# Optimization experiments

Measured on AMD Instinct MI355X. Metric: run time of the kernel, lower is better.

Reference implementation:

```python
import jax
import jax.numpy as jnp
from jax import lax
import numpy as np

B, N, NPOINT, NSAMPLE, C = 8, 8192, 2048, 32, 64
RADIUS = 0.2
BIG = jnp.float32(1e10)


def setup_inputs() -> dict:
    key = jax.random.key(0)
    ks = jax.random.split(key, 8)
    xyz = jax.random.uniform(ks[0], (B, N, 3), dtype=jnp.float32)          # points in unit cube
    features = jax.random.normal(ks[1], (B, C, N), dtype=jnp.float32)
    w1 = jax.random.normal(ks[2], (64, C + 3), dtype=jnp.float32) * 0.1
    b1 = jnp.zeros((64,), jnp.float32)
    w2 = jax.random.normal(ks[3], (64, 64), dtype=jnp.float32) * 0.1
    b2 = jnp.zeros((64,), jnp.float32)
    w3 = jax.random.normal(ks[4], (128, 64), dtype=jnp.float32) * 0.1
    b3 = jnp.zeros((128,), jnp.float32)
    return {"xyz": xyz, "features": features, "w1": w1, "b1": b1,
            "w2": w2, "b2": b2, "w3": w3, "b3": b3}


def _fps(xyz, npoint):
    """Furthest point sampling. xyz: (B,N,3) -> idx (B,npoint) int32."""
    def one(pts):  # (N,3)
        n = pts.shape[0]
        def step(carry, _):
            dist, far = carry
            d = jnp.sum((pts - pts[far]) ** 2, axis=-1)    # (N,)
            dist = jnp.minimum(dist, d)
            nxt = jnp.argmax(dist).astype(jnp.int32)
            return (dist, nxt), far
        init = (jnp.full((n,), BIG, pts.dtype), jnp.int32(0))
        _, idx = lax.scan(step, init, None, length=npoint)
        return idx
    return jax.vmap(one)(xyz)


def _ball_query(xyz, new_xyz, radius, nsample):
    """xyz (B,N,3), new_xyz (B,S,3) -> idx (B,S,nsample) int32, pointnet2 semantics:
    first nsample in-radius points in index order; pad with first hit."""
    n = xyz.shape[1]
    d2 = (jnp.sum(new_xyz ** 2, -1)[:, :, None]
          + jnp.sum(xyz ** 2, -1)[:, None, :]
          - 2.0 * jnp.einsum("bsd,bnd->bsn", new_xyz, xyz))  # (B,S,N)
    mask = d2 < radius * radius
    keys = jnp.where(mask, jnp.arange(n, dtype=jnp.int32)[None, None, :], jnp.int32(n))
    idx = jnp.sort(keys, axis=-1)[..., :nsample]             # (B,S,nsample)
    first = idx[..., :1]
    idx = jnp.where(idx >= n, first, idx)
    idx = jnp.where(idx >= n, 0, idx)                        # degenerate: no neighbor at all
    return idx


def _conv_bn_relu(h, w, b):
    # 1x1 Conv2d over (B, Cin, S, ns) with folded BN -> ReLU
    return jax.nn.relu(jnp.einsum("oc,bcps->bops", w, h) + b[None, :, None, None])


def _forward(xyz, features, w1, b1, w2, b2, w3, b3):
    fps_idx = _fps(xyz, NPOINT)                                          # (B,S)
    new_xyz = jnp.take_along_axis(xyz, fps_idx[:, :, None], axis=1)      # (B,S,3)
    idx = _ball_query(xyz, new_xyz, RADIUS, NSAMPLE)                     # (B,S,ns)
    b, s, ns = idx.shape
    flat = idx.reshape(b, s * ns)
    grouped_xyz = jnp.take_along_axis(xyz, flat[:, :, None], axis=1).reshape(b, s, ns, 3)
    grouped_xyz = grouped_xyz - new_xyz[:, :, None, :]                   # center
    grouped_xyz = jnp.transpose(grouped_xyz, (0, 3, 1, 2))               # (B,3,S,ns)
    grouped_feat = jnp.take_along_axis(features, flat[:, None, :], axis=2).reshape(b, C, s, ns)
    h = jnp.concatenate([grouped_xyz, grouped_feat], axis=1)             # (B,3+C,S,ns)
    h = _conv_bn_relu(h, w1, b1)
    h = _conv_bn_relu(h, w2, b2)
    h = _conv_bn_relu(h, w3, b3)
    new_features = jnp.max(h, axis=-1)                                   # (B,128,S)
    return new_xyz, new_features


def reference(xyz, features, w1, b1, w2, b2, w3, b3):
    return _forward(xyz, features, w1, b1, w2, b2, w3, b3)
```

## Files before the change

### kernel.cpp

```cpp
#include <hip/hip_runtime.h>
#include <stdint.h>

#define NB 8
#define NN 8192
#define NP 2048
#define NSAMP 32
#define NC 64

__global__ __launch_bounds__(256) void prep_kernel(
    const float* __restrict__ w1, const float* __restrict__ w2,
    const float* __restrict__ w3, float* __restrict__ w1t,
    float* __restrict__ w2t, float* __restrict__ w3t)
{
    int j = blockIdx.x * 256 + threadIdx.x;
    if (j < 64*67) { int o = j / 67, k = j % 67; w1t[k*64 + o] = w1[j]; }
    int j2 = j - 64*67;
    if (j2 >= 0 && j2 < 64*64) { int o = j2 >> 6, k = j2 & 63; w2t[k*64 + o] = w2[j2]; }
    int j3 = j2 - 64*64;
    if (j3 >= 0 && j3 < 128*64) { int o = j3 >> 6, k = j3 & 63; w3t[k*128 + o] = w3[j3]; }
}

#define DPP_MAXF(m, CTRL) do { \
    int _s = __builtin_amdgcn_update_dpp(__float_as_int(m), __float_as_int(m), \
                                         CTRL, 0xf, 0xf, false); \
    float _f = __int_as_float(_s); \
    m = fmaxf(m, _f); } while (0)

#define DPP_MINI(c, CTRL) do { \
    int _s = __builtin_amdgcn_update_dpp(c, c, CTRL, 0xf, 0xf, false); \
    c = (_s < c) ? _s : c; } while (0)

__global__ __launch_bounds__(256, 1) void fps_kernel(
    const float* __restrict__ xyz, int* __restrict__ fps_idx,
    float* __restrict__ out_newxyz)
{
#pragma clang fp contract(off)
    __shared__ float sxyz[NN * 3];
    __shared__ float bv[2][4];
    __shared__ int   bix[2][4];

    const int b = blockIdx.x;
    const int t = threadIdx.x;
    const int lane = t & 63;
    const int w = t >> 6;
    const float* base = xyz + (size_t)b * NN * 3;

    for (int i = t; i < NN * 3 / 4; i += 256)
        ((float4*)sxyz)[i] = ((const float4*)base)[i];
    __syncthreads();

    const int p0 = t * 32;
    float px[32], py[32], pz[32], dist[32];
    #pragma unroll
    for (int j = 0; j < 32; j++) {
        px[j] = sxyz[(p0 + j) * 3 + 0];
        py[j] = sxyz[(p0 + j) * 3 + 1];
        pz[j] = sxyz[(p0 + j) * 3 + 2];
        dist[j] = 1e10f;
    }

    int far = 0;
    for (int k = 0; k < NP; k++) {
        float fx = sxyz[far * 3 + 0];
        float fy = sxyz[far * 3 + 1];
        float fz = sxyz[far * 3 + 2];
        if (t == 0) {
            fps_idx[b * NP + k] = far;
            out_newxyz[((size_t)b * NP + k) * 3 + 0] = fx;
            out_newxyz[((size_t)b * NP + k) * 3 + 1] = fy;
            out_newxyz[((size_t)b * NP + k) * 3 + 2] = fz;
        }

        float bva0 = -1.f, bva1 = -1.f, bva2 = -1.f, bva3 = -1.f;
        int   bja0 = 0,    bja1 = 0,    bja2 = 0,    bja3 = 0;
        #pragma unroll
        for (int j8 = 0; j8 < 8; j8++) {
            {   int j = j8;
                float dx = px[j] - fx, dy = py[j] - fy, dz = pz[j] - fz;
                float d = (dx*dx + dy*dy) + dz*dz;
                float nd = fminf(dist[j], d); dist[j] = nd;
                if (nd > bva0) { bva0 = nd; bja0 = p0 + j; } }
            {   int j = 8 + j8;
                float dx = px[j] - fx, dy = py[j] - fy, dz = pz[j] - fz;
                float d = (dx*dx + dy*dy) + dz*dz;
                float nd = fminf(dist[j], d); dist[j] = nd;
                if (nd > bva1) { bva1 = nd; bja1 = p0 + j; } }
            {   int j = 16 + j8;
                float dx = px[j] - fx, dy = py[j] - fy, dz = pz[j] - fz;
                float d = (dx*dx + dy*dy) + dz*dz;
                float nd = fminf(dist[j], d); dist[j] = nd;
                if (nd > bva2) { bva2 = nd; bja2 = p0 + j; } }
            {   int j = 24 + j8;
                float dx = px[j] - fx, dy = py[j] - fy, dz = pz[j] - fz;
                float d = (dx*dx + dy*dy) + dz*dz;
                float nd = fminf(dist[j], d); dist[j] = nd;
                if (nd > bva3) { bva3 = nd; bja3 = p0 + j; } }
        }
        float best = bva0; int bj = bja0;
        if (bva1 > best) { best = bva1; bj = bja1; }
        if (bva2 > best) { best = bva2; bj = bja2; }
        if (bva3 > best) { best = bva3; bj = bja3; }

        float m = best;
        DPP_MAXF(m, 0x111); DPP_MAXF(m, 0x112); DPP_MAXF(m, 0x114);
        DPP_MAXF(m, 0x118); DPP_MAXF(m, 0x142); DPP_MAXF(m, 0x143);
        float wm = __int_as_float(__builtin_amdgcn_readlane(__float_as_int(m), 63));

        int cand = (best == wm) ? bj : 0x7FFFFFFF;
        DPP_MINI(cand, 0x111); DPP_MINI(cand, 0x112); DPP_MINI(cand, 0x114);
        DPP_MINI(cand, 0x118); DPP_MINI(cand, 0x142); DPP_MINI(cand, 0x143);
        int widx = __builtin_amdgcn_readlane(cand, 63);

        if (lane == 0) { bv[k & 1][w] = wm; bix[k & 1][w] = widx; }
        __syncthreads();

        float v0 = bv[k & 1][0], v1 = bv[k & 1][1];
        float v2 = bv[k & 1][2], v3 = bv[k & 1][3];
        int   i0 = bix[k & 1][0], i1 = bix[k & 1][1];
        int   i2 = bix[k & 1][2], i3 = bix[k & 1][3];
        float gv = v0; int gi = i0;
        if (v1 > gv) { gv = v1; gi = i1; }
        if (v2 > gv) { gv = v2; gi = i2; }
        if (v3 > gv) { gv = v3; gi = i3; }
        far = gi;
    }
}

__global__ __launch_bounds__(64) void fused_kernel(
    const float* __restrict__ xyz, const float* __restrict__ features,
    const int* __restrict__ fps_idx,
    const float* __restrict__ w1t, const float* __restrict__ b1,
    const float* __restrict__ w2t, const float* __restrict__ b2,
    const float* __restrict__ w3t, const float* __restrict__ b3,
    float* __restrict__ out_feat)
{
#pragma clang fp contract(off)
    constexpr int XP = 36;
    __shared__ __align__(16) float Xs[67 * XP];
    __shared__ __align__(16) float Hs[64 * XP];
    __shared__ int ids[NSAMP];

    const int q = blockIdx.x;
    const int b = q >> 11, s = q & (NP - 1);
    const int lane = threadIdx.x;
    const float* base = xyz + (size_t)b * NN * 3;

    int qi = fps_idx[q];
    float qx = base[qi*3+0], qy = base[qi*3+1], qz = base[qi*3+2];
    float qq = (qx*qx + qy*qy) + qz*qz;
    const float RR = 0.04f;

    int have = 0, first = 0;
    for (int c = 0; c < NN / 64; c++) {
        int p = c * 64 + lane;
        float px = base[p*3+0], py = base[p*3+1], pz = base[p*3+2];
        float pp  = (px*px + py*py) + pz*pz;
        float dot = fmaf(qz, pz, fmaf(qy, py, qx*px));
        float d2  = (qq + pp) - 2.0f*dot;
        bool pred = d2 < RR;
        unsigned long long m = __ballot(pred);
        if (have == 0 && m) first = c * 64 + (int)__builtin_ctzll(m);
        if (pred) {
            int rank = have + (int)__popcll(m & ((1ULL << lane) - 1ULL));
            if (rank < NSAMP) ids[rank] = p;
        }
        have += (int)__popcll(m);
        if (have >= NSAMP) break;
    }
    if (lane < NSAMP && lane >= have) ids[lane] = first;
    __syncthreads();

    if (lane < NSAMP) {
        int id = ids[lane];
        Xs[0*XP + lane] = base[id*3+0] - qx;
        Xs[1*XP + lane] = base[id*3+1] - qy;
        Xs[2*XP + lane] = base[id*3+2] - qz;
    }
    {
        const float* frow = features + ((size_t)b * NC + lane) * NN;
        #pragma unroll
        for (int n0 = 0; n0 < NSAMP; n0 += 4) {
            float4 v;
            v.x = frow[ids[n0+0]];
            v.y = frow[ids[n0+1]];
            v.z = frow[ids[n0+2]];
            v.w = frow[ids[n0+3]];
            *(float4*)&Xs[(3 + lane) * XP + n0] = v;
        }
    }
    __syncthreads();

    float acc[32];
    {
        float bias = b1[lane];
        #pragma unroll
        for (int n = 0; n < 32; n++) acc[n] = bias;
        for (int k = 0; k < 67; k++) {
            float w = w1t[k*64 + lane];
            const float4* xr = (const float4*)&Xs[k * XP];
            #pragma unroll
            for (int n4 = 0; n4 < 8; n4++) {
                float4 xv = xr[n4];
                acc[n4*4+0] = fmaf(w, xv.x, acc[n4*4+0]);
                acc[n4*4+1] = fmaf(w, xv.y, acc[n4*4+1]);
                acc[n4*4+2] = fmaf(w, xv.z, acc[n4*4+2]);
                acc[n4*4+3] = fmaf(w, xv.w, acc[n4*4+3]);
            }
        }
        #pragma unroll
        for (int n0 = 0; n0 < 32; n0 += 4) {
            float4 v;
            v.x = fmaxf(acc[n0+0], 0.f); v.y = fmaxf(acc[n0+1], 0.f);
            v.z = fmaxf(acc[n0+2], 0.f); v.w = fmaxf(acc[n0+3], 0.f);
            *(float4*)&Hs[lane * XP + n0] = v;
        }
    }
    __syncthreads();
    {
        float bias = b2[lane];
        #pragma unroll
        for (int n = 0; n < 32; n++) acc[n] = bias;
        for (int k = 0; k < 64; k++) {
            float w = w2t[k*64 + lane];
            const float4* xr = (const float4*)&Hs[k * XP];
            #pragma unroll
            for (int n4 = 0; n4 < 8; n4++) {
                float4 xv = xr[n4];
                acc[n4*4+0] = fmaf(w, xv.x, acc[n4*4+0]);
                acc[n4*4+1] = fmaf(w, xv.y, acc[n4*4+1]);
                acc[n4*4+2] = fmaf(w, xv.z, acc[n4*4+2]);
                acc[n4*4+3] = fmaf(w, xv.w, acc[n4*4+3]);
            }
        }
        __syncthreads();
        #pragma unroll
        for (int n0 = 0; n0 < 32; n0 += 4) {
            float4 v;
            v.x = fmaxf(acc[n0+0], 0.f); v.y = fmaxf(acc[n0+1], 0.f);
            v.z = fmaxf(acc[n0+2], 0.f); v.w = fmaxf(acc[n0+3], 0.f);
            *(float4*)&Xs[lane * XP + n0] = v;
        }
    }
    __syncthreads();
    {
        float accA[32], accB[32];
        float ba = b3[lane], bb = b3[lane + 64];
        #pragma unroll
        for (int n = 0; n < 32; n++) { accA[n] = ba; accB[n] = bb; }
        for (int k = 0; k < 64; k++) {
            float wa = w3t[k*128 + lane];
            float wb = w3t[k*128 + lane + 64];
            const float4* xr = (const float4*)&Xs[k * XP];
            #pragma unroll
            for (int n4 = 0; n4 < 8; n4++) {
                float4 xv = xr[n4];
                accA[n4*4+0] = fmaf(wa, xv.x, accA[n4*4+0]);
                accA[n4*4+1] = fmaf(wa, xv.y, accA[n4*4+1]);
                accA[n4*4+2] = fmaf(wa, xv.z, accA[n4*4+2]);
                accA[n4*4+3] = fmaf(wa, xv.w, accA[n4*4+3]);
                accB[n4*4+0] = fmaf(wb, xv.x, accB[n4*4+0]);
                accB[n4*4+1] = fmaf(wb, xv.y, accB[n4*4+1]);
                accB[n4*4+2] = fmaf(wb, xv.z, accB[n4*4+2]);
                accB[n4*4+3] = fmaf(wb, xv.w, accB[n4*4+3]);
            }
        }
        float mA = accA[0], mB = accB[0];
        #pragma unroll
        for (int n = 1; n < 32; n++) { mA = fmaxf(mA, accA[n]); mB = fmaxf(mB, accB[n]); }
        mA = fmaxf(mA, 0.f); mB = fmaxf(mB, 0.f);
        out_feat[((size_t)b*128 + lane)      * NP + s] = mA;
        out_feat[((size_t)b*128 + lane + 64) * NP + s] = mB;
    }
}

extern "C" void kernel_launch(void* const* d_in, const int* in_sizes, int n_in,
                              void* d_out, int out_size, void* d_ws, size_t ws_size,
                              hipStream_t stream)
{
    const float* xyz      = (const float*)d_in[0];
    const float* features = (const float*)d_in[1];
    const float* w1 = (const float*)d_in[2];
    const float* b1 = (const float*)d_in[3];
    const float* w2 = (const float*)d_in[4];
    const float* b2 = (const float*)d_in[5];
    const float* w3 = (const float*)d_in[6];
    const float* b3 = (const float*)d_in[7];

    float* out        = (float*)d_out;
    float* out_newxyz = out;
    float* out_feat   = out + NB * NP * 3;

    char* ws = (char*)d_ws;
    int*   fps_idx = (int*)(ws + 0);
    float* w1t     = (float*)(ws + 65536);
    float* w2t     = (float*)(ws + 82688);
    float* w3t     = (float*)(ws + 99072);

    prep_kernel<<<65, 256, 0, stream>>>(w1, w2, w3, w1t, w2t, w3t);
    fps_kernel<<<NB, 256, 0, stream>>>(xyz, fps_idx, out_newxyz);
    fused_kernel<<<NB * NP, 64, 0, stream>>>(xyz, features, fps_idx,
                                             w1t, b1, w2t, b2, w3t, b3, out_feat);
}
```

Measured before the change: 2.382 ms.

## Widen FPS block to 512 threads with packed float2 math and max-then-find argmax

The furthest point sampling kernel now runs 512 threads per block, each owning 16 points instead of 32, which halves the serial per-iteration work in this latency-bound loop. Coordinates and distances are held as two-wide float vectors so the distance computation can use packed FP32 instructions. The per-thread argmax is split into a plain max reduction followed by an equality scan for the lowest matching index. The cost is a cross-wave reduction over 8 waves instead of 4, and the block barrier per iteration now synchronises more waves.

```diff
diff --git a/kernel.cpp b/kernel.cpp
--- a/kernel.cpp
+++ b/kernel.cpp
@@ -6,6 +6,8 @@
 #define NP 2048
 #define NSAMP 32
 #define NC 64
+
+typedef float v2f __attribute__((ext_vector_type(2)));
 
 __global__ __launch_bounds__(256) void prep_kernel(
     const float* __restrict__ w1, const float* __restrict__ w2,
@@ -30,14 +32,14 @@
     int _s = __builtin_amdgcn_update_dpp(c, c, CTRL, 0xf, 0xf, false); \
     c = (_s < c) ? _s : c; } while (0)
 
-__global__ __launch_bounds__(256, 1) void fps_kernel(
+__global__ __launch_bounds__(512) void fps_kernel(
     const float* __restrict__ xyz, int* __restrict__ fps_idx,
     float* __restrict__ out_newxyz)
 {
 #pragma clang fp contract(off)
     __shared__ float sxyz[NN * 3];
-    __shared__ float bv[2][4];
-    __shared__ int   bix[2][4];
+    __shared__ float bv[2][8];
+    __shared__ int   bix[2][8];
 
     const int b = blockIdx.x;
     const int t = threadIdx.x;
@@ -45,18 +47,19 @@
     const int w = t >> 6;
     const float* base = xyz + (size_t)b * NN * 3;
 
-    for (int i = t; i < NN * 3 / 4; i += 256)
+    for (int i = t; i < NN * 3 / 4; i += 512)
         ((float4*)sxyz)[i] = ((const float4*)base)[i];
     __syncthreads();
 
-    const int p0 = t * 32;
-    float px[32], py[32], pz[32], dist[32];
+    const int p0 = t * 16;
+    v2f X[8], Y[8], Z[8], D[8];
     #pragma unroll
-    for (int j = 0; j < 32; j++) {
-        px[j] = sxyz[(p0 + j) * 3 + 0];
-        py[j] = sxyz[(p0 + j) * 3 + 1];
-        pz[j] = sxyz[(p0 + j) * 3 + 2];
-        dist[j] = 1e10f;
+    for (int j = 0; j < 8; j++) {
+        int pa = p0 + 2*j, pb = p0 + 2*j + 1;
+        X[j] = (v2f){ sxyz[pa*3+0], sxyz[pb*3+0] };
+        Y[j] = (v2f){ sxyz[pa*3+1], sxyz[pb*3+1] };
+        Z[j] = (v2f){ sxyz[pa*3+2], sxyz[pb*3+2] };
+        D[j] = (v2f){ 1e10f, 1e10f };
     }
 
     int far = 0;
@@ -71,42 +74,35 @@
             out_newxyz[((size_t)b * NP + k) * 3 + 2] = fz;
         }
 
-        float bva0 = -1.f, bva1 = -1.f, bva2 = -1.f, bva3 = -1.f;
-        int   bja0 = 0,    bja1 = 0,    bja2 = 0,    bja3 = 0;
-        #pragma unroll
-        for (int j8 = 0; j8 < 8; j8++) {
-            {   int j = j8;
-                float dx = px[j] - fx, dy = py[j] - fy, dz = pz[j] - fz;
-                float d = (dx*dx + dy*dy) + dz*dz;
-                float nd = fminf(dist[j], d); dist[j] = nd;
-                if (nd > bva0) { bva0 = nd; bja0 = p0 + j; } }
-            {   int j = 8 + j8;
-                float dx = px[j] - fx, dy = py[j] - fy, dz = pz[j] - fz;
-                float d = (dx*dx + dy*dy) + dz*dz;
-                float nd = fminf(dist[j], d); dist[j] = nd;
-                if (nd > bva1) { bva1 = nd; bja1 = p0 + j; } }
-            {   int j = 16 + j8;
-                float dx = px[j] - fx, dy = py[j] - fy, dz = pz[j] - fz;
-                float d = (dx*dx + dy*dy) + dz*dz;
-                float nd = fminf(dist[j], d); dist[j] = nd;
-                if (nd > bva2) { bva2 = nd; bja2 = p0 + j; } }
-            {   int j = 24 + j8;
-                float dx = px[j] - fx, dy = py[j] - fy, dz = pz[j] - fz;
-                float d = (dx*dx + dy*dy) + dz*dz;
-                float nd = fminf(dist[j], d); dist[j] = nd;
-                if (nd > bva3) { bva3 = nd; bja3 = p0 + j; } }
-        }
-        float best = bva0; int bj = bja0;
-        if (bva1 > best) { best = bva1; bj = bja1; }
-        if (bva2 > best) { best = bva2; bj = bja2; }
-        if (bva3 > best) { best = bva3; bj = bja3; }
-
-        float m = best;
+        v2f fx2 = { fx, fx }, fy2 = { fy, fy }, fz2 = { fz, fz };
+        #pragma unroll
+        for (int j = 0; j < 8; j++) {
+            v2f dx = X[j] - fx2;
+            v2f dy = Y[j] - fy2;
+            v2f dz = Z[j] - fz2;
+            v2f d  = (dx*dx + dy*dy) + dz*dz;
+            D[j].x = fminf(D[j].x, d.x);
+            D[j].y = fminf(D[j].y, d.y);
+        }
+
+        float m0 = fmaxf(fmaxf(D[0].x, D[0].y), D[1].x);
+        float m1 = fmaxf(fmaxf(D[1].y, D[2].x), D[2].y);
+        float m2 = fmaxf(fmaxf(D[3].x, D[3].y), D[4].x);
+        float m3 = fmaxf(fmaxf(D[4].y, D[5].x), D[5].y);
+        float m4 = fmaxf(fmaxf(D[6].x, D[6].y), D[7].x);
+        float m  = fmaxf(fmaxf(fmaxf(m0, m1), fmaxf(m2, m3)),
+                         fmaxf(m4, D[7].y));
+
         DPP_MAXF(m, 0x111); DPP_MAXF(m, 0x112); DPP_MAXF(m, 0x114);
         DPP_MAXF(m, 0x118); DPP_MAXF(m, 0x142); DPP_MAXF(m, 0x143);
         float wm = __int_as_float(__builtin_amdgcn_readlane(__float_as_int(m), 63));
 
-        int cand = (best == wm) ? bj : 0x7FFFFFFF;
+        int cand = 0x7FFFFFFF;
+        #pragma unroll
+        for (int j = 7; j >= 0; j--) {
+            if (D[j].y == wm) cand = p0 + 2*j + 1;
+            if (D[j].x == wm) cand = p0 + 2*j;
+        }
         DPP_MINI(cand, 0x111); DPP_MINI(cand, 0x112); DPP_MINI(cand, 0x114);
         DPP_MINI(cand, 0x118); DPP_MINI(cand, 0x142); DPP_MINI(cand, 0x143);
         int widx = __builtin_amdgcn_readlane(cand, 63);
@@ -114,14 +110,12 @@
         if (lane == 0) { bv[k & 1][w] = wm; bix[k & 1][w] = widx; }
         __syncthreads();
 
-        float v0 = bv[k & 1][0], v1 = bv[k & 1][1];
-        float v2 = bv[k & 1][2], v3 = bv[k & 1][3];
-        int   i0 = bix[k & 1][0], i1 = bix[k & 1][1];
-        int   i2 = bix[k & 1][2], i3 = bix[k & 1][3];
-        float gv = v0; int gi = i0;
-        if (v1 > gv) { gv = v1; gi = i1; }
-        if (v2 > gv) { gv = v2; gi = i2; }
-        if (v3 > gv) { gv = v3; gi = i3; }
+        float gv = bv[k & 1][0]; int gi = bix[k & 1][0];
+        #pragma unroll
+        for (int ww = 1; ww < 8; ww++) {
+            float v = bv[k & 1][ww]; int i = bix[k & 1][ww];
+            if (v > gv) { gv = v; gi = i; }
+        }
         far = gi;
     }
 }
@@ -297,7 +291,7 @@
     float* w3t     = (float*)(ws + 99072);
 
     prep_kernel<<<65, 256, 0, stream>>>(w1, w2, w3, w1t, w2t, w3t);
-    fps_kernel<<<NB, 256, 0, stream>>>(xyz, fps_idx, out_newxyz);
+    fps_kernel<<<NB, 512, 0, stream>>>(xyz, fps_idx, out_newxyz);
     fused_kernel<<<NB * NP, 64, 0, stream>>>(xyz, features, fps_idx,
                                              w1t, b1, w2t, b2, w3t, b3, out_feat);
 }
```

Result: slower. 2.538 ms (+6.5%).
